# Optimization experiments

Hardware: AMD Instinct MI355X
Metric: run time of the kernel (lower is better)

## Reference

```python
import jax, jax.numpy as jnp
import numpy as np

BETA = 0.25
N_E = 8192
E_DIM = 256


def setup_inputs() -> dict:
    key = jax.random.key(0)
    k1, k2 = jax.random.split(key)
    z = jax.random.normal(k1, (16, E_DIM, 32, 32), dtype=jnp.float32)
    # matches torch init: uniform_(-1/n_e, 1/n_e)
    codebook = jax.random.uniform(k2, (N_E, E_DIM), dtype=jnp.float32,
                                  minval=-1.0 / N_E, maxval=1.0 / N_E)
    return {"z": z, "codebook": codebook}


def reference(z, codebook):
    B, C, H, W = z.shape  # C == e_dim
    zp = jnp.transpose(z, (0, 2, 3, 1))          # [B, H, W, C]
    zf = zp.reshape(-1, C)                       # [N, C], N = B*H*W
    # squared L2 distances: ||z||^2 + ||e||^2 - 2 z.e
    d = (jnp.sum(zf * zf, axis=1, keepdims=True)
         + jnp.sum(codebook * codebook, axis=1)
         - 2.0 * jnp.einsum('nc,kc->nk', zf, codebook))  # [N, n_e]
    min_encoding_indices = jnp.argmin(d, axis=1)         # [N]
    z_q = codebook[min_encoding_indices].reshape(zp.shape)  # [B, H, W, C]
    sg = jax.lax.stop_gradient
    loss = jnp.mean((sg(z_q) - zp) ** 2) + BETA * jnp.mean((z_q - sg(zp)) ** 2)
    # straight-through estimator
    z_q_st = zp + sg(z_q - zp)
    z_q_out = jnp.transpose(z_q_st, (0, 3, 1, 2))  # back to NCHW
    return z_q_out, loss, min_encoding_indices
```

## Files before the change

kernel.cpp:

```cpp
#include <hip/hip_runtime.h>

typedef short s8v __attribute__((ext_vector_type(8)));
typedef float f4v __attribute__((ext_vector_type(4)));
typedef float f4 __attribute__((ext_vector_type(4)));

#define N_PIX 16384
#define NE    8192
#define EDIM  256
#define ZQ_ELEMS 4194304
#define MARGIN 4.5e-4f
#define NGRP 512

__device__ __forceinline__ float bf2f(unsigned short u) {
    union { unsigned int i; float f; } c; c.i = ((unsigned int)u) << 16; return c.f;
}
__device__ __forceinline__ unsigned short f2bf(float f) {
    unsigned int u = __float_as_uint(f);
    u = (u + 0x7fffu + ((u >> 16) & 1u)) >> 16;
    return (unsigned short)u;
}
__device__ __forceinline__ unsigned short f2bf_down(float f) {
    unsigned int u = __float_as_uint(f);
    unsigned short b = (unsigned short)(u >> 16);
    if ((u & 0xFFFFu) && (u >> 31)) b += 1;
    return b;
}

__device__ __forceinline__ float np_pw128sq(const float* a) {
    float r[8];
    #pragma unroll
    for (int j = 0; j < 8; ++j) r[j] = __fmul_rn(a[j], a[j]);
    for (int i = 8; i < 128; i += 8)
        #pragma unroll
        for (int j = 0; j < 8; ++j) r[j] = __fadd_rn(r[j], __fmul_rn(a[i + j], a[i + j]));
    return __fadd_rn(__fadd_rn(__fadd_rn(r[0], r[1]), __fadd_rn(r[2], r[3])),
                     __fadd_rn(__fadd_rn(r[4], r[5]), __fadd_rn(r[6], r[7])));
}

__global__ __launch_bounds__(256) void vq_prep(const float* __restrict__ cb,
                                               unsigned short* __restrict__ cb16,
                                               float* __restrict__ esum32) {
    int t = threadIdx.x;
    int base = blockIdx.x * 64;
    const float* src = cb + (size_t)base * EDIM;
    unsigned short* dst = cb16 + (size_t)base * EDIM;
    for (int i = 0; i < 64; ++i) dst[i * EDIM + t] = f2bf(src[i * EDIM + t]);
    if (t < 64) {
        const float* a = cb + (size_t)(base + t) * EDIM;
        esum32[base + t] = __fadd_rn(np_pw128sq(a), np_pw128sq(a + 128));
    }
}

__global__ __launch_bounds__(256) void vq_zprep(const float* __restrict__ z,
                                                unsigned short* __restrict__ z16) {
    __shared__ unsigned short zl[64 * 66];
    int t = threadIdx.x;
    int p0 = (blockIdx.x >> 2) * 64;
    int c0 = (blockIdx.x & 3) * 64;
    int b = p0 >> 10, hw0 = p0 & 1023;
    const float* src = z + (((size_t)b * 256 + c0) << 10) + hw0;
    #pragma unroll
    for (int i = 0; i < 16; ++i) {
        int idx = i * 256 + t;
        int ch = idx >> 6, px = idx & 63;
        zl[px * 66 + ch] = f2bf(src[((size_t)ch << 10) + px]);
    }
    __syncthreads();
    #pragma unroll
    for (int i = 0; i < 16; ++i) {
        int idx = i * 256 + t;
        int px = idx >> 6, ch = idx & 63;
        z16[((size_t)(p0 + px)) * 256 + c0 + ch] = zl[px * 66 + ch];
    }
}

__global__ __launch_bounds__(512, 2) void vq_phase1g(const unsigned short* __restrict__ cb16,
                                                     const unsigned short* __restrict__ z16,
                                                     unsigned short* __restrict__ gmin) {
    __shared__ unsigned short L[2][32768];
    const int t = threadIdx.x;
    const int wave = t >> 6, lane = t & 63;
    const int q = lane >> 4, r = lane & 15;
    const int wr = wave >> 2, wc = wave & 3;
    const int cm0 = ((int)blockIdx.x >> 3) * 256;
    const int pg  = (int)blockIdx.x & 7;

    const int pc0 = t, pc1 = t + 512;
    const int row0 = pc0 >> 2, row1 = pc1 >> 2;
    const int lc0 = (pc0 & 3) ^ ((row0 >> 1) & 3);
    const int lc1 = (pc1 & 3) ^ ((row1 >> 1) & 3);
    const int go0 = row0 * 256 + lc0 * 8;
    const int go1 = row1 * 256 + lc1 * 8;
    const int ld0 = pc0 * 8;
    const int ld1 = pc1 * 8;

    const unsigned short* gA = cb16 + (size_t)cm0 * 256;
    const unsigned short* gB0 = z16 + (size_t)pg * 2048 * 256;

    f4v acc[8][4];
    const f4v zz = {0.f, 0.f, 0.f, 0.f};
    #pragma unroll
    for (int mi = 0; mi < 8; ++mi)
        #pragma unroll
        for (int ni = 0; ni < 4; ++ni) acc[mi][ni] = zz;

    const int cxo = (q ^ ((r >> 1) & 3)) * 8;
    const int aro = (wr * 128 + r) * 32 + cxo;
    const int bro = 16384 + (wc * 64 + r) * 32 + cxo;

#define GLL(g, l) __builtin_amdgcn_global_load_lds( \
        (const __attribute__((address_space(1))) unsigned int*)(g), \
        (__attribute__((address_space(3))) unsigned int*)(l), 16, 0, 0)
#define STAGEKT(buf_, gk_, gBp_) do { \
        unsigned short* Lb = &L[(buf_)][0]; \
        GLL(gA + go0 + (gk_),            Lb + ld0); \
        GLL(gA + go1 + (gk_),            Lb + ld1); \
        GLL(gA + go0 + 32 + (gk_),       Lb + 8192 + ld0); \
        GLL(gA + go1 + 32 + (gk_),       Lb + 8192 + ld1); \
        GLL((gBp_) + go0 + (gk_),        Lb + 16384 + ld0); \
        GLL((gBp_) + go1 + (gk_),        Lb + 16384 + ld1); \
        GLL((gBp_) + go0 + 32 + (gk_),   Lb + 16384 + 8192 + ld0); \
        GLL((gBp_) + go1 + 32 + (gk_),   Lb + 16384 + 8192 + ld1); } while (0)
#define ARD(Lp, mi, ks) (*(const s8v*)&(Lp)[(ks) * 8192 + (mi) * 512 + aro])
#define BRD(Lp, ni, ks) (*(const s8v*)&(Lp)[(ks) * 8192 + (ni) * 512 + bro])
#define MFMA16(Aset, Bset, mo) do { \
        __builtin_amdgcn_s_setprio(1); \
        _Pragma("unroll") \
        for (int mi = 0; mi < 4; ++mi) \
            _Pragma("unroll") \
            for (int ni = 0; ni < 4; ++ni) \
                acc[(mo) + mi][ni] = __builtin_amdgcn_mfma_f32_16x16x32_bf16( \
                    Aset[mi], Bset[ni], acc[(mo) + mi][ni], 0, 0, 0); \
        __builtin_amdgcn_s_setprio(0); } while (0)

    STAGEKT(0, 0, gB0);
    asm volatile("s_waitcnt vmcnt(0)" ::: "memory");
    __builtin_amdgcn_s_barrier();
    s8v A0[4], A1[4], B0[4], B1[4];
    #pragma unroll
    for (int ni = 0; ni < 4; ++ni) B0[ni] = BRD(&L[0][0], ni, 0);
    #pragma unroll
    for (int mi = 0; mi < 4; ++mi) A0[mi] = ARD(&L[0][0], mi, 0);

    for (int it = 0; it < 32; ++it) {
        const int buf = it & 1;
        const unsigned short* Lb = &L[buf][0];
        const unsigned short* Ln = &L[buf ^ 1][0];
        const int nit = it + 1;
        const bool st = nit < 32;

        __builtin_amdgcn_s_barrier();
        if (st) STAGEKT(buf ^ 1, (nit & 3) * 64, gB0 + (size_t)(nit >> 2) * 65536);

        #pragma unroll
        for (int mi = 0; mi < 4; ++mi) A1[mi] = ARD(Lb, 4 + mi, 0);
        __builtin_amdgcn_sched_barrier(0);
        MFMA16(A0, B0, 0);

        #pragma unroll
        for (int mi = 0; mi < 4; ++mi) A0[mi] = ARD(Lb, mi, 1);
        #pragma unroll
        for (int ni = 0; ni < 4; ++ni) B1[ni] = BRD(Lb, ni, 1);
        __builtin_amdgcn_sched_barrier(0);
        MFMA16(A1, B0, 4);

        #pragma unroll
        for (int mi = 0; mi < 4; ++mi) A1[mi] = ARD(Lb, 4 + mi, 1);
        __builtin_amdgcn_sched_barrier(0);
        MFMA16(A0, B1, 0);

        if (st) {
            asm volatile("s_waitcnt vmcnt(0)" ::: "memory");
            __builtin_amdgcn_s_barrier();
            #pragma unroll
            for (int ni = 0; ni < 4; ++ni) B0[ni] = BRD(Ln, ni, 0);
            #pragma unroll
            for (int mi = 0; mi < 4; ++mi) A0[mi] = ARD(Ln, mi, 0);
        }
        __builtin_amdgcn_sched_barrier(0);
        MFMA16(A1, B1, 4);

        if ((it & 3) == 3) {
            const int pn0 = pg * 2048 + (it >> 2) * 256;
            #pragma unroll
            for (int mi = 0; mi < 8; ++mi) {
                int g = cm0 / 16 + wr * 8 + mi;
                #pragma unroll
                for (int ni = 0; ni < 4; ++ni) {
                    f4v a = acc[mi][ni];
                    float mx = fmaxf(fmaxf(a[0], a[1]), fmaxf(a[2], a[3]));
                    mx = fmaxf(mx, __shfl_xor(mx, 16));
                    mx = fmaxf(mx, __shfl_xor(mx, 32));
                    if (q == 0)
                        gmin[(size_t)g * N_PIX + pn0 + wc * 64 + ni * 16 + r] =
                            f2bf_down(-2.0f * mx);
                    acc[mi][ni] = zz;
                }
            }
        }
    }
#undef MFMA16
#undef BRD
#undef ARD
#undef STAGEKT
#undef GLL
}

__global__ __launch_bounds__(512, 2) void vq_phase1(const float* __restrict__ z,
                                                    const unsigned short* __restrict__ cb16,
                                                    unsigned short* __restrict__ gmin) {
    const int t = threadIdx.x;
    const int wave = t >> 6, lane = t & 63;
    const int col = lane & 15, q = lane >> 4;
    const int mb = (blockIdx.x >> 1) * 64;
    const int chalf = blockIdx.x & 1;

    s8v Z[4][8];
    #pragma unroll
    for (int pt = 0; pt < 4; ++pt) {
        int n = mb + pt * 16 + col;
        const float* zb = z + ((size_t)(n >> 10) << 18) + (size_t)(n & 1023);
        #pragma unroll
        for (int c0 = 0; c0 < 8; ++c0) {
            s8v a;
            #pragma unroll
            for (int j = 0; j < 8; ++j) {
                int c = c0 * 32 + q * 8 + j;
                a[j] = (short)f2bf(zb[(size_t)c << 10]);
            }
            Z[pt][c0] = a;
        }
    }

    const int kbase = chalf * 4096 + wave * 512;
    for (int it = 0; it < 16; ++it) {
        int n0 = kbase + it * 32;
        const unsigned short* bb = cb16 + (size_t)(n0 + col) * EDIM + q * 8;
        f4v zz = {0.f, 0.f, 0.f, 0.f};
        f4v acc[4][2];
        #pragma unroll
        for (int pt = 0; pt < 4; ++pt) { acc[pt][0] = zz; acc[pt][1] = zz; }
        #pragma unroll
        for (int c0 = 0; c0 < 8; ++c0) {
            s8v C0 = *(const s8v*)(bb + c0 * 32);
            s8v C1 = *(const s8v*)(bb + 16 * EDIM + c0 * 32);
            #pragma unroll
            for (int pt = 0; pt < 4; ++pt) {
                acc[pt][0] = __builtin_amdgcn_mfma_f32_16x16x32_bf16(C0, Z[pt][c0], acc[pt][0], 0, 0, 0);
                acc[pt][1] = __builtin_amdgcn_mfma_f32_16x16x32_bf16(C1, Z[pt][c0], acc[pt][1], 0, 0, 0);
            }
        }
        int gbase = chalf * 256 + wave * 32 + it * 2;
        #pragma unroll
        for (int pt = 0; pt < 4; ++pt) {
            #pragma unroll
            for (int s = 0; s < 2; ++s) {
                f4v a = acc[pt][s];
                float mx = fmaxf(fmaxf(a[0], a[1]), fmaxf(a[2], a[3]));
                mx = fmaxf(mx, __shfl_xor(mx, 16));
                mx = fmaxf(mx, __shfl_xor(mx, 32));
                if (q == 0)
                    gmin[(size_t)(gbase + s) * N_PIX + mb + pt * 16 + col] =
                        f2bf_down(-2.0f * mx);
            }
        }
    }
}

__global__ __launch_bounds__(256) void vq_phase2(const float* __restrict__ z,
                                                 const float* __restrict__ cb,
                                                 const float* __restrict__ esum32,
                                                 const unsigned short* __restrict__ gmin,
                                                 unsigned int* __restrict__ idxw) {
    __shared__ float zt[16 * 260];
    __shared__ unsigned short gm[NGRP * 17];
    __shared__ float zs[16];
    int t = threadIdx.x;
    int wave = t >> 6, lane = t & 63;
    int p0 = blockIdx.x * 16;
    int bb = p0 >> 10, inner = p0 & 1023;

    #pragma unroll
    for (int i = 0; i < 16; ++i) {
        int c = i * 16 + (t >> 4), p = t & 15;
        zt[p * 260 + c] = z[((size_t)(bb * 256 + c) << 10) + inner + p];
    }
    #pragma unroll
    for (int i = 0; i < 32; ++i) {
        int g = i * 16 + (t >> 4), p = t & 15;
        gm[g * 17 + p] = gmin[(size_t)g * N_PIX + p0 + p];
    }
    __syncthreads();
    if (t < 16) {
        const float* a = zt + t * 260;
        zs[t] = __fadd_rn(np_pw128sq(a), np_pw128sq(a + 128));
    }
    __syncthreads();

    #pragma unroll
    for (int pp = 0; pp < 4; ++pp) {
        int p = wave * 4 + pp;
        float lmin = 3.0e38f;
        #pragma unroll
        for (int j = 0; j < 8; ++j) lmin = fminf(lmin, bf2f(gm[(lane * 8 + j) * 17 + p]));
        #pragma unroll
        for (int m = 1; m < 64; m <<= 1) lmin = fminf(lmin, __shfl_xor(lmin, m));
        float thr = lmin + MARGIN;
        float zsp = zs[p];

        float bd = 3.0e38f; int bk = 0x7FFFFFFF;
        for (int j = 0; j < 8; ++j) {
            unsigned long long mask = __ballot(bf2f(gm[(lane * 8 + j) * 17 + p]) <= thr);
            while (mask) {
                int lb = __builtin_ctzll(mask); mask &= mask - 1;
                int g = lb * 8 + j;
                int k = g * 16 + (lane >> 2);
                const f4* cr = (const f4*)(cb + (size_t)k * EDIM) + (lane & 3);
                const f4* zr = (const f4*)(zt + p * 260) + (lane & 3);
                double a0 = 0.0, a1 = 0.0, a2 = 0.0, a3 = 0.0;
                #pragma unroll
                for (int i = 0; i < 16; ++i) {
                    f4 x = zr[i * 4], y = cr[i * 4];
                    a0 = fma((double)x[0], (double)y[0], a0);
                    a1 = fma((double)x[1], (double)y[1], a1);
                    a2 = fma((double)x[2], (double)y[2], a2);
                    a3 = fma((double)x[3], (double)y[3], a3);
                }
                double s = (a0 + a1) + (a2 + a3);
                s += __shfl_xor(s, 1);
                s += __shfl_xor(s, 2);
                float E = (float)s;
                float d = __fsub_rn(__fadd_rn(zsp, esum32[k]), __fmul_rn(2.0f, E));
                if (d < bd || (d == bd && k < bk)) { bd = d; bk = k; }
            }
        }
        #pragma unroll
        for (int m = 1; m < 64; m <<= 1) {
            float od = __shfl_xor(bd, m); int ok = __shfl_xor(bk, m);
            if (od < bd || (od == bd && ok < bk)) { bd = od; bk = ok; }
        }
        if (lane == 0) idxw[p0 + p] = (unsigned int)bk;
    }
}

__global__ __launch_bounds__(256) void vq_emit(const float* __restrict__ cb,
                                               const float* __restrict__ z,
                                               const unsigned int* __restrict__ idxw,
                                               float* __restrict__ outf,
                                               float* __restrict__ lossw) {
    __shared__ float red[4];
    int t = threadIdx.x;
    int gtid = blockIdx.x * 256 + t;
    if (gtid < N_PIX) outf[ZQ_ELEMS + 1 + gtid] = (float)(idxw[gtid] & (NE - 1));

    float acc = 0.f;
    size_t base = (size_t)blockIdx.x * 16384;
    for (int i = 0; i < 64; ++i) {
        size_t o = base + (size_t)i * 256 + t;
        int b = (int)(o >> 18);
        int c = (int)((o >> 10) & 255);
        int p = (int)(o & 1023);
        int idx = (int)(idxw[b * 1024 + p] & (NE - 1));
        float qv = cb[(size_t)idx * EDIM + c];
        outf[o] = qv;
        float d = qv - z[o];
        acc = fmaf(d, d, acc);
    }
    #pragma unroll
    for (int off = 32; off > 0; off >>= 1) acc += __shfl_down(acc, off);
    if ((t & 63) == 0) red[t >> 6] = acc;
    __syncthreads();
    if (t == 0) atomicAdd(lossw, red[0] + red[1] + red[2] + red[3]);
}

__global__ void vq_finalize(const float* __restrict__ lossw, float* __restrict__ loss_out) {
    loss_out[0] = 1.25f * lossw[0] * (1.0f / 4194304.0f);
}

extern "C" void kernel_launch(void* const* d_in, const int* in_sizes, int n_in,
                              void* d_out, int out_size, void* d_ws, size_t ws_size,
                              hipStream_t stream) {
    const float* z  = (const float*)d_in[0];
    const float* cb = (const float*)d_in[1];
    float* outf = (float*)d_out;
    unsigned short* gmin = (unsigned short*)d_out;

    char* w = (char*)d_ws;
    unsigned short* cb16   = (unsigned short*)w;
    float*          esum32 = (float*)(w + 4194304);
    unsigned int*   idxw   = (unsigned int*)(w + 4227072);
    float*          lossw  = (float*)(w + 4292608);
    unsigned short* z16    = (unsigned short*)(w + 4292864);

    if (ws_size < 4292612) return;
    const bool big_ws = (ws_size >= 12681472);

    hipMemsetAsync(lossw, 0, sizeof(float), stream);
    vq_prep    <<<NE / 64, 256, 0, stream>>>(cb, cb16, esum32);
    if (big_ws) {
        vq_zprep  <<<(N_PIX / 64) * (EDIM / 64), 256, 0, stream>>>(z, z16);
        vq_phase1g<<<(NE / 256) * (N_PIX / 2048), 512, 0, stream>>>(cb16, z16, gmin);
    } else {
        vq_phase1 <<<(N_PIX / 64) * 2, 512, 0, stream>>>(z, cb16, gmin);
    }
    vq_phase2  <<<N_PIX / 16, 256, 0, stream>>>(z, cb, esum32, gmin, idxw);
    vq_emit    <<<256, 256, 0, stream>>>(cb, z, idxw, outf, lossw);
    vq_finalize<<<1, 1, 0, stream>>>(lossw, outf + ZQ_ELEMS);
}
```

Baseline: 276.7 us.

## Reorganize gmin layout, vectorize codebook prep, stage gathered codebook rows in emit

Changes the group-min buffer to a pixel-chunk-major layout so phase2 can read each block's 8192 entries contiguously with 16-byte loads instead of strided 2-byte loads. The codebook bf16 conversion now uses float4 loads and packed 4x16-bit stores with twice as many blocks. The emit kernel gathers the selected codebook rows for a 16-channel slice into padded shared memory once, replacing per-element scattered global gathers. Shared-memory use in emit rises to about 74 KB, which may reduce occupancy.

Result: faster. 263.8 us (-4.7%).

```diff
diff --git a/kernel.cpp b/kernel.cpp
--- a/kernel.cpp
+++ b/kernel.cpp
@@ -3,6 +3,7 @@
 typedef short s8v __attribute__((ext_vector_type(8)));
 typedef float f4v __attribute__((ext_vector_type(4)));
 typedef float f4 __attribute__((ext_vector_type(4)));
+typedef unsigned short u16v4 __attribute__((ext_vector_type(4)));
 
 #define N_PIX 16384
 #define NE    8192
@@ -37,15 +38,23 @@
                      __fadd_rn(__fadd_rn(r[4], r[5]), __fadd_rn(r[6], r[7])));
 }
 
+
 __global__ __launch_bounds__(256) void vq_prep(const float* __restrict__ cb,
                                                unsigned short* __restrict__ cb16,
                                                float* __restrict__ esum32) {
     int t = threadIdx.x;
-    int base = blockIdx.x * 64;
+    int base = blockIdx.x * 32;
     const float* src = cb + (size_t)base * EDIM;
     unsigned short* dst = cb16 + (size_t)base * EDIM;
-    for (int i = 0; i < 64; ++i) dst[i * EDIM + t] = f2bf(src[i * EDIM + t]);
-    if (t < 64) {
+    #pragma unroll
+    for (int i = 0; i < 8; ++i) {
+        int e0 = (i * 256 + t) * 4;
+        f4 v = *(const f4*)(src + e0);
+        u16v4 o;
+        o.x = f2bf(v[0]); o.y = f2bf(v[1]); o.z = f2bf(v[2]); o.w = f2bf(v[3]);
+        *(u16v4*)(dst + e0) = o;
+    }
+    if (t < 32) {
         const float* a = cb + (size_t)(base + t) * EDIM;
         esum32[base + t] = __fadd_rn(np_pw128sq(a), np_pw128sq(a + 128));
     }
@@ -191,9 +200,10 @@
                     float mx = fmaxf(fmaxf(a[0], a[1]), fmaxf(a[2], a[3]));
                     mx = fmaxf(mx, __shfl_xor(mx, 16));
                     mx = fmaxf(mx, __shfl_xor(mx, 32));
-                    if (q == 0)
-                        gmin[(size_t)g * N_PIX + pn0 + wc * 64 + ni * 16 + r] =
-                            f2bf_down(-2.0f * mx);
+                    if (q == 0) {
+                        int pxc = (pn0 + wc * 64 + ni * 16) >> 4;
+                        gmin[(size_t)pxc * 8192 + g * 16 + r] = f2bf_down(-2.0f * mx);
+                    }
                     acc[mi][ni] = zz;
                 }
             }
@@ -260,7 +270,7 @@
                 mx = fmaxf(mx, __shfl_xor(mx, 16));
                 mx = fmaxf(mx, __shfl_xor(mx, 32));
                 if (q == 0)
-                    gmin[(size_t)(gbase + s) * N_PIX + mb + pt * 16 + col] =
+                    gmin[(size_t)((mb >> 4) + pt) * 8192 + (gbase + s) * 16 + col] =
                         f2bf_down(-2.0f * mx);
             }
         }
@@ -285,10 +295,14 @@
         int c = i * 16 + (t >> 4), p = t & 15;
         zt[p * 260 + c] = z[((size_t)(bb * 256 + c) << 10) + inner + p];
     }
-    #pragma unroll
-    for (int i = 0; i < 32; ++i) {
-        int g = i * 16 + (t >> 4), p = t & 15;
-        gm[g * 17 + p] = gmin[(size_t)g * N_PIX + p0 + p];
+    const unsigned short* gsrc = gmin + (size_t)blockIdx.x * 8192;
+    #pragma unroll
+    for (int j = 0; j < 4; ++j) {
+        int li = (j * 256 + t) * 8;
+        s8v v = *(const s8v*)(gsrc + li);
+        int g = li >> 4, ph = li & 15;
+        #pragma unroll
+        for (int e = 0; e < 8; ++e) gm[g * 17 + ph + e] = (unsigned short)v[e];
     }
     __syncthreads();
     if (t < 16) {
@@ -348,20 +362,36 @@
                                                const unsigned int* __restrict__ idxw,
                                                float* __restrict__ outf,
                                                float* __restrict__ lossw) {
+    __shared__ float qrow[1024 * 17];
+    __shared__ unsigned int lidx[1024];
     __shared__ float red[4];
     int t = threadIdx.x;
     int gtid = blockIdx.x * 256 + t;
     if (gtid < N_PIX) outf[ZQ_ELEMS + 1 + gtid] = (float)(idxw[gtid] & (NE - 1));
 
+    int b = blockIdx.x >> 4;
+    int c0 = (blockIdx.x & 15) * 16;
+
+    #pragma unroll
+    for (int j = 0; j < 4; ++j)
+        lidx[j * 256 + t] = idxw[b * 1024 + j * 256 + t] & (NE - 1);
+    __syncthreads();
+    #pragma unroll
+    for (int j = 0; j < 16; ++j) {
+        int p = j * 64 + (t >> 2);
+        f4 v = *(const f4*)(cb + (size_t)lidx[p] * EDIM + c0 + (t & 3) * 4);
+        #pragma unroll
+        for (int e = 0; e < 4; ++e) qrow[p * 17 + (t & 3) * 4 + e] = v[e];
+    }
+    __syncthreads();
+
     float acc = 0.f;
     size_t base = (size_t)blockIdx.x * 16384;
     for (int i = 0; i < 64; ++i) {
         size_t o = base + (size_t)i * 256 + t;
-        int b = (int)(o >> 18);
         int c = (int)((o >> 10) & 255);
         int p = (int)(o & 1023);
-        int idx = (int)(idxw[b * 1024 + p] & (NE - 1));
-        float qv = cb[(size_t)idx * EDIM + c];
+        float qv = qrow[p * 17 + (c - c0)];
         outf[o] = qv;
         float d = qv - z[o];
         acc = fmaf(d, d, acc);
@@ -396,7 +426,7 @@
     const bool big_ws = (ws_size >= 12681472);
 
     hipMemsetAsync(lossw, 0, sizeof(float), stream);
-    vq_prep    <<<NE / 64, 256, 0, stream>>>(cb, cb16, esum32);
+    vq_prep    <<<NE / 32, 256, 0, stream>>>(cb, cb16, esum32);
     if (big_ws) {
         vq_zprep  <<<(N_PIX / 64) * (EDIM / 64), 256, 0, stream>>>(z, z16);
         vq_phase1g<<<(NE / 256) * (N_PIX / 2048), 512, 0, stream>>>(cb16, z16, gmin);
```
